# Kernel tuning notes

Hardware: AMD Instinct MI355X
Metric: run time of the kernel (lower is better)

Reference implementation:

```python
import jax, jax.numpy as jnp
import numpy as np


def _l2norm(x, axis):
    return x / jnp.maximum(jnp.linalg.norm(x, axis=axis, keepdims=True), 1e-12)


def setup_inputs() -> dict:
    key = jax.random.key(0)
    ks = jax.random.split(key, 16)
    N, D, F, TI, HD = 1000, 100, 100, 512, 128
    # binary doc-word membership masks, ~50 words per document
    masks = (jax.random.uniform(ks[0], (D, N)) < 0.05).astype(jnp.float32)
    # sparse symmetric normalized word-graph adjacency
    a = (jax.random.uniform(ks[1], (N, N)) < 0.01).astype(jnp.float32)
    adj = jnp.maximum(a, a.T) + jnp.eye(N, dtype=jnp.float32)
    dinv = 1.0 / jnp.sqrt(adj.sum(axis=1))
    train_adj = adj * dinv[:, None] * dinv[None, :]
    bows_vec = jax.random.normal(ks[2], (N, F), dtype=jnp.float32) * 0.1
    image_features = jax.random.normal(ks[3], (D, TI), dtype=jnp.float32)

    def sc(i, sh):
        return jax.random.normal(ks[i], sh, dtype=jnp.float32) * np.float32(1.0 / np.sqrt(sh[0]))

    return {
        'epoch': 3, 'epochs': 10,
        'train_adj': train_adj, 'masks': masks, 'bows_vec': bows_vec,
        'image_features': image_features,
        'W_g1': sc(4, (F, F)), 'W_g2': sc(5, (F, F)),
        'W_h1': sc(6, (F, F)), 'b_h1': jnp.zeros(F, jnp.float32),
        'W_h2': sc(7, (F, F)), 'b_h2': jnp.zeros(F, jnp.float32),
        'W_mu2': sc(8, (F, 1)), 'b_mu2': jnp.zeros(1, jnp.float32),
        'W_eta2': sc(9, (F, 1)), 'b_eta2': jnp.zeros(1, jnp.float32),
        'W_gamma2': sc(10, (F, 1)), 'b_gamma2': jnp.zeros(1, jnp.float32),
        'w_m': sc(11, (F, 1)), 'W_beta': sc(12, (F, 1)),
        'W_m1': sc(13, (TI, HD)), 'b_m1': jnp.zeros(HD, jnp.float32),
        'W_m2': sc(14, (HD, 1)), 'b_m2': jnp.zeros(1, jnp.float32),
    }


def reference(epoch, epochs, train_adj, masks, bows_vec, image_features,
              W_g1, W_g2, W_h1, b_h1, W_h2, b_h2,
              W_mu2, b_mu2, W_eta2, b_eta2, W_gamma2, b_gamma2,
              w_m, W_beta, W_m1, b_m1, W_m2, b_m2):
    N = train_adj.shape[0]
    # --- GcnNet: 2-layer GCN over word graph; doc embedding = masked mean pool ---
    H1 = jax.nn.relu(train_adj @ (bows_vec @ W_g1))        # [N,100]
    H = train_adj @ (H1 @ W_g2)                            # [N,100]
    cnt = masks.sum(axis=1, keepdims=True)                 # [D,1]
    H_p = (masks @ H) / jnp.maximum(cnt, 1.0)              # [D,100]

    H_eli = jax.nn.relu(jax.nn.relu(H @ W_h1 + b_h1) @ W_h2 + b_h2)
    H_eli_norm = _l2norm(H_eli, axis=1)                    # [N,100]

    mu = jax.nn.relu(H_p @ W_mu2 + b_mu2)                  # [D,1]
    # dropout disabled (eval mode)
    eta = jax.nn.relu(H_p @ W_eta2 + b_eta2)               # [D,1]
    gamma = jax.nn.relu(H_p @ W_gamma2 + b_gamma2)         # [D,1]

    sparsity = (epoch / epochs) * 0.3                      # python float (static)
    flat = w_m.reshape(-1)
    j = int(round(sparsity * flat.shape[0]))
    order = jnp.argsort(flat)                              # ascending; drop lowest j
    binary = jnp.zeros_like(flat).at[order[j:]].set(1.0)
    mask_ste = flat + jax.lax.stop_gradient(binary - flat) # forward==binary
    w_pruned = mask_ste.reshape(-1, 1) * W_beta            # [100,1]
    beta_ = _l2norm((H @ w_pruned)[:, 0], axis=0)          # [N]
    beta = masks @ beta_[:, None]                          # [D,1]

    Z_ = jax.nn.relu(H_eli_norm @ H_eli_norm.T)            # [N,N]

    # per-doc sum over distinct word pairs of h_i . h_j ; ||h||=1 so
    # sum_{a<b} h_a.h_b = (||sum_a h_a||^2 - k)/2 with k = #words in doc
    s = masks @ H_eli_norm                                 # [D,100]
    k = masks.sum(axis=1)                                  # [D]
    Z = jax.nn.relu(0.5 * (jnp.sum(s * s, axis=1) - k))[:, None]  # [D,1]

    # Z_event: per-doc [N,N] with entries at local positions p,q < k_i (p!=q)
    # (original indexes Z_ with LOCAL sorted positions 0..k_i-1; kept faithful)
    pos = jnp.arange(N)
    valid = (pos[None, :] < k[:, None]).astype(jnp.float32)       # [D,N]
    E = jnp.exp(-jnp.square(2.0 - 2.0 * Z_)) * (1.0 - jnp.eye(N)) # [N,N]
    Z_event = E[None, :, :] * valid[:, :, None] * valid[:, None, :]  # [D,N,N]

    lambda_texts = jax.nn.sigmoid(mu + beta + eta * jnp.exp(-gamma * Z))
    h_img = jax.nn.relu(image_features @ W_m1 + b_m1)
    lambda_imgs = h_img @ W_m2 + b_m2                      # MLP(512,128,1)
    lambda_total = jax.nn.sigmoid(lambda_texts + lambda_imgs)
    return (lambda_total, Z_, beta_, gamma, eta, Z_event, H)
```

## Files before the change

kernel.cpp:

```cpp
#include <hip/hip_runtime.h>
#include <hip/hip_bf16.h>

typedef __hip_bfloat16 bf;

#define NN   1000
#define DD   100
#define FF   100
#define TIF  512
#define HDD  128
#define EB   256
#define ACAP 96
#define MCAP 192

#define O_LAM 0
#define O_Z   100
#define O_B3  1000100
#define O_GAM 1001100
#define O_ETA 1001200
#define O_ZE  1001300
#define O_H   101001300

__device__ __forceinline__ float ldf(const void* p, int i, int F32){
  return F32 ? ((const float*)p)[i] : __bfloat162float(((const __hip_bfloat16*)p)[i]);
}

__device__ __forceinline__ float blk_red(float v, volatile float* red, int tid){
#pragma unroll
  for (int o=32;o>0;o>>=1) v += __shfl_down(v,o,64);
  if ((tid&63)==0) red[tid>>6]=v;
  __syncthreads();
  float r = red[0]+red[1];
  __syncthreads();
  return r;
}
__device__ __forceinline__ float blk_red4(float v, volatile float* red, int tid){
#pragma unroll
  for (int o=32;o>0;o>>=1) v += __shfl_down(v,o,64);
  if ((tid&63)==0) red[tid>>6]=v;
  __syncthreads();
  float r = red[0]+red[1]+red[2]+red[3];
  __syncthreads();
  return r;
}

__device__ __forceinline__ int sniffF32(const unsigned short* __restrict__ p, int tid){
  int lane = tid & 63;
  const ushort4* q = (const ushort4*)p;
  ushort4 a = q[lane*2], b = q[lane*2+1];
  int c = 0;
  c += (((a.x>>7)&0xFF)>=0xE0); c += (((a.y>>7)&0xFF)>=0xE0);
  c += (((a.z>>7)&0xFF)>=0xE0); c += (((a.w>>7)&0xFF)>=0xE0);
  c += (((b.x>>7)&0xFF)>=0xE0); c += (((b.y>>7)&0xFF)>=0xE0);
  c += (((b.z>>7)&0xFF)>=0xE0); c += (((b.w>>7)&0xFF)>=0xE0);
#pragma unroll
  for (int o=32;o>0;o>>=1) c += __shfl_xor(c,o,64);
  return c > 8;
}

__device__ __forceinline__ void zero_span(uint4* __restrict__ zb, long off, long cnt,
                                          int zi, int nzb, int tid, int bdim){
  long per = (cnt + nzb - 1)/nzb;
  long s = (long)zi*per; if (s>cnt) s=cnt;
  long e = s+per; if (e>cnt) e=cnt;
  uint4 z; z.x=z.y=z.z=z.w=0u;
  for (long i=off+s+tid; i<off+e; i+=bdim) zb[i]=z;
}

__global__ void k1_build(const void* __restrict__ A, const void* __restrict__ masks,
                         const void* __restrict__ wm, const void* __restrict__ Wbeta,
                         const void* __restrict__ img, const void* __restrict__ Wm1,
                         const void* __restrict__ bm1, const void* __restrict__ Wm2,
                         const void* __restrict__ bm2, const void* __restrict__ X,
                         const void* __restrict__ Wg1,
                         const int* epoch, const int* epochs,
                         int* a_idx, float* a_val, int* a_nnz,
                         int* m_idx, int* m_cnt, float* wpr, float* sumsq,
                         float* limg, int* flag, float* __restrict__ XW,
                         uint4* __restrict__ zb){
  int b = blockIdx.x; int lane = threadIdx.x;
  if (b >= NN+DD+1+DD+NN){ zero_span(zb, 0L, 8000000L, b-(NN+DD+1+DD+NN), 2048, lane, 64); return; }
  int F32 = sniffF32((const unsigned short*)X, lane);
  if (b < NN){
    int i=b, nn=0;
    for (int base=0;base<NN;base+=64){
      int c=base+lane; float v=0.f;
      if (c<NN) v=ldf(A, i*NN+c, F32);
      unsigned long long m=__ballot(v!=0.f);
      if (v!=0.f){
        int pos=nn+__popcll(m&((1ull<<lane)-1ull));
        if (pos<ACAP){ a_idx[i*ACAP+pos]=c; a_val[i*ACAP+pos]=v; }
      }
      nn+=__popcll(m);
    }
    if (lane==0) a_nnz[i]=min(nn,ACAP);
  } else if (b < NN+DD){
    int d=b-NN, nn=0;
    for (int base=0;base<NN;base+=64){
      int c=base+lane; float v=0.f;
      if (c<NN) v=ldf(masks, d*NN+c, F32);
      unsigned long long m=__ballot(v!=0.f);
      if (v!=0.f){
        int pos=nn+__popcll(m&((1ull<<lane)-1ull));
        if (pos<MCAP) m_idx[d*MCAP+pos]=c;
      }
      nn+=__popcll(m);
    }
    if (lane==0) m_cnt[d]=min(nn,MCAP);
  } else if (b == NN+DD){
    __shared__ float w[FF];
    for (int t=lane;t<FF;t+=64) w[t]=ldf(wm, t, F32);
    __syncthreads();
    float sp = 0.3f*(float)epoch[0]/(float)epochs[0];
    int j=(int)lroundf(sp*(float)FF);
    for (int t=lane;t<FF;t+=64){
      float v=w[t]; int r=0;
      for (int u=0;u<FF;u++){ float vu=w[u]; r += ((vu<v)||(vu==v && u<t)) ? 1 : 0; }
      wpr[t] = (r>=j)? ldf(Wbeta, t, F32) : 0.f;
    }
    if (lane==0){ sumsq[0]=0.f; flag[0]=F32; }
  } else if (b < NN+DD+1+DD){
    int d = b - (NN+DD+1);
    __shared__ float ir[TIF];
    for (int t=lane;t<TIF;t+=64) ir[t]=ldf(img, d*TIF+t, F32);
    __syncthreads();
    float acc=0.f;
    for (int h=lane; h<HDD; h+=64){
      float a=ldf(bm1, h, F32);
#pragma unroll 4
      for (int t=0;t<TIF;t++) a=fmaf(ir[t], ldf(Wm1, t*HDD+h, F32), a);
      acc = fmaf(fmaxf(a,0.f), ldf(Wm2, h, F32), acc);
    }
#pragma unroll
    for (int o=32;o>0;o>>=1) acc += __shfl_down(acc,o,64);
    if (lane==0) limg[d]=acc+ldf(bm2,0,F32);
  } else {
    int r = b - (NN+DD+1+DD);
    __shared__ float ar[FF];
    for (int t=lane;t<FF;t+=64) ar[t]=ldf(X, r*FF+t, F32);
    __syncthreads();
    for (int col=lane; col<FF; col+=64){
      float a=0.f;
#pragma unroll 4
      for (int c=0;c<FF;c++) a=fmaf(ar[c], ldf(Wg1, c*FF+col, F32), a);
      XW[r*FF+col]=a;
    }
  }
}

__global__ void k2_h1(const float* __restrict__ XW, const void* __restrict__ Wg2,
                      const int* flag, const int* __restrict__ a_idx,
                      const float* __restrict__ a_val, const int* __restrict__ a_nnz,
                      float* __restrict__ H1W, uint4* __restrict__ zb){
  int row=blockIdx.x, tx=threadIdx.x;
  if (row >= NN){ zero_span(zb, 8000000L, 5000000L, row-NN, 1280, tx, 128); return; }
  __shared__ int sidx[ACAP]; __shared__ float sval[ACAP]; __shared__ float t1[FF];
  int nn=a_nnz[row];
  for (int t=tx;t<nn;t+=128){ sidx[t]=a_idx[row*ACAP+t]; sval[t]=a_val[row*ACAP+t]; }
  __syncthreads();
  if (tx<FF){
    float a=0.f;
    for (int m=0;m<nn;m++) a=fmaf(sval[m], XW[sidx[m]*FF+tx], a);
    t1[tx]=fmaxf(a,0.f);
  }
  __syncthreads();
  int F32=flag[0];
  if (tx<FF){
    float s=0.f;
#pragma unroll 4
    for (int c=0;c<FF;c++) s=fmaf(t1[c], ldf(Wg2, c*FF+tx, F32), s);
    H1W[row*FF+tx]=s;
  }
}

__global__ void k3_h2(const float* __restrict__ H1W, const int* __restrict__ a_idx,
                      const float* __restrict__ a_val, const int* __restrict__ a_nnz,
                      const void* __restrict__ Wh1, const void* __restrict__ bh1,
                      const void* __restrict__ Wh2, const void* __restrict__ bh2,
                      const float* __restrict__ wpr, const int* flag,
                      float* __restrict__ Hh, float* __restrict__ Hn,
                      float* __restrict__ HnT, float* __restrict__ hw, float* sumsq,
                      float* __restrict__ outH, uint4* __restrict__ zb){
  int i=blockIdx.x, tx=threadIdx.x;
  if (i >= NN){ zero_span(zb, 13000000L, 5000000L, i-NN, 1280, tx, 128); return; }
  __shared__ int sidx[ACAP]; __shared__ float sval[ACAP];
  __shared__ float hr[FF], t1[FF];
  __shared__ float red[2];
  int nn=a_nnz[i];
  for (int t=tx;t<nn;t+=128){ sidx[t]=a_idx[i*ACAP+t]; sval[t]=a_val[i*ACAP+t]; }
  __syncthreads();
  if (tx<FF){
    float a=0.f;
    for (int m=0;m<nn;m++) a=fmaf(sval[m], H1W[sidx[m]*FF+tx], a);
    hr[tx]=a; Hh[i*FF+tx]=a; outH[i*FF+tx]=a;
  }
  __syncthreads();
  int F32=flag[0];
  if (tx<FF){
    float a=ldf(bh1, tx, F32);
#pragma unroll 4
    for (int c=0;c<FF;c++) a=fmaf(hr[c], ldf(Wh1, c*FF+tx, F32), a);
    t1[tx]=fmaxf(a,0.f);
  }
  __syncthreads();
  float hel=0.f;
  if (tx<FF){
    float s=ldf(bh2, tx, F32);
#pragma unroll 4
    for (int c=0;c<FF;c++) s=fmaf(t1[c], ldf(Wh2, c*FF+tx, F32), s);
    hel=fmaxf(s,0.f);
  }
  float phw = (tx<FF)? hr[tx]*wpr[tx] : 0.f;
  float rs2 = blk_red(hel*hel, red, tx);
  float rhw = blk_red(phw, red, tx);
  float rinv = 1.f/fmaxf(sqrtf(rs2), 1e-12f);
  if (tx<FF){ float v=hel*rinv; Hn[i*FF+tx]=v; HnT[tx*NN+i]=v; }
  if (tx==0){ hw[i]=rhw; atomicAdd(sumsq, rhw*rhw); }
}

__global__ __launch_bounds__(256) void k4_zdoc(const float* __restrict__ HnT,
                      const float* __restrict__ Hh, const float* __restrict__ Hn,
                      const float* __restrict__ hw, const float* __restrict__ sumsq,
                      const int* __restrict__ m_idx, const int* __restrict__ m_cnt,
                      const void* Wmu, const void* bmu, const void* Weta, const void* beta_b,
                      const void* Wgam, const void* bgam, const int* flag,
                      const float* __restrict__ limg,
                      float* __restrict__ out, float* __restrict__ Eblk,
                      uint4* __restrict__ zb){
  int b=blockIdx.x, tid=threadIdx.x;
  if (b >= 360){ zero_span(zb, 18000000L, 7000000L, b-360, 1792, tid, 256); return; }
  if (b < 256){
    int bi=(b&15)*64, bj=(b>>4)*64;
    __shared__ float At[FF*68], Bt[FF*68];
    for (int t=tid;t<FF*64;t+=256){
      int k=t>>6, ii=t&63;
      int gi=bi+ii, gj=bj+ii;
      At[k*68+ii] = (gi<NN)? HnT[k*NN+gi] : 0.f;
      Bt[k*68+ii] = (gj<NN)? HnT[k*NN+gj] : 0.f;
    }
    __syncthreads();
    int tx=tid&15, ty=tid>>4;
    float acc[4][4]={};
    for (int k=0;k<FF;k++){
      float4 av=*(float4*)&At[k*68+4*ty];
      float4 bv=*(float4*)&Bt[k*68+4*tx];
      float aa[4]={av.x,av.y,av.z,av.w};
      float bb[4]={bv.x,bv.y,bv.z,bv.w};
#pragma unroll
      for (int q=0;q<4;q++)
#pragma unroll
        for (int r=0;r<4;r++) acc[q][r]=fmaf(aa[q],bb[r],acc[q][r]);
    }
#pragma unroll
    for (int q=0;q<4;q++){
      int gi=bi+4*ty+q; if (gi>=NN) continue;
      float z[4];
#pragma unroll
      for (int r=0;r<4;r++) z[r]=fmaxf(acc[q][r],0.f);
      int gj0=bj+4*tx;
      if (gj0+3<NN){
        float4 zz; zz.x=z[0]; zz.y=z[1]; zz.z=z[2]; zz.w=z[3];
        *(float4*)&out[O_Z+(size_t)gi*NN+gj0]=zz;
      } else {
        for (int r=0;r<4;r++) if (gj0+r<NN) out[O_Z+(size_t)gi*NN+gj0+r]=z[r];
      }
      if (gi<EB && gj0<EB){
#pragma unroll
        for (int r=0;r<4;r++){
          int gj=gj0+r;
          float t2=2.f-2.f*z[r];
          Eblk[gi*EB+gj]=(gi==gj)?0.f:expf(-t2*t2);
        }
      }
    }
    return;
  }
  if (b >= 356){
    int i=(b-356)*256+tid;
    if (i<NN){
      float rinv=1.f/fmaxf(sqrtf(sumsq[0]),1e-12f);
      out[O_B3+i]=hw[i]*rinv;
    }
    return;
  }
  int d=b-256;
  int F32 = flag[0];
  __shared__ int sidx[MCAP]; __shared__ float red[4];
  int cnt=m_cnt[d];
  for (int t=tid;t<cnt;t+=256) sidx[t]=m_idx[d*MCAP+t];
  __syncthreads();
  float accH=0.f, accS=0.f;
  if (tid<FF) for (int m=0;m<cnt;m++){ int n=sidx[m]; accH+=Hh[n*FF+tid]; accS+=Hn[n*FF+tid]; }
  float Hp = accH/fmaxf((float)cnt,1.f);
  float pmu = (tid<FF)? Hp*ldf(Wmu, tid, F32)  : 0.f;
  float peta= (tid<FF)? Hp*ldf(Weta, tid, F32) : 0.f;
  float pgam= (tid<FF)? Hp*ldf(Wgam, tid, F32) : 0.f;
  float phw=0.f;
  for (int m=tid;m<cnt;m+=256) phw+=hw[sidx[m]];
  float rmu =blk_red4(pmu,red,tid);
  float reta=blk_red4(peta,red,tid);
  float rgam=blk_red4(pgam,red,tid);
  float rs2 =blk_red4(accS*accS,red,tid);
  float rhw =blk_red4(phw,red,tid);
  if (tid==0){
    float mu =fmaxf(rmu +ldf(bmu,0,F32),   0.f);
    float eta=fmaxf(reta+ldf(beta_b,0,F32),0.f);
    float gam=fmaxf(rgam+ldf(bgam,0,F32),  0.f);
    float Zd =fmaxf(0.5f*(rs2-(float)cnt), 0.f);
    float beta=rhw/fmaxf(sqrtf(sumsq[0]),1e-12f);
    float lt=1.f/(1.f+expf(-(mu+beta+eta*expf(-gam*Zd))));
    out[O_LAM+d]=1.f/(1.f+expf(-(lt+limg[d])));
    out[O_GAM+d]=gam;
    out[O_ETA+d]=eta;
  }
}

__global__ void k5_fill(const float* __restrict__ Eblk, const int* __restrict__ m_cnt,
                        float* __restrict__ outZE){
  int d=blockIdx.x; int k=m_cnt[d]; if (k>EB) k=EB;
  int kk=k*k;
  for (int idx=threadIdx.x; idx<kk; idx+=256){
    int i=idx/k, j=idx-i*k;
    float e=(i==j)?0.f:Eblk[i*EB+j];
    outZE[(size_t)d*1000000 + (size_t)i*1000 + j]=e;
  }
}

extern "C" void kernel_launch(void* const* d_in, const int* in_sizes, int n_in,
                              void* d_out, int out_size, void* d_ws, size_t ws_size,
                              hipStream_t stream) {
  const int* epoch  = (const int*)d_in[0];
  const int* epochs = (const int*)d_in[1];
  const void* A     = d_in[2];
  const void* masks = d_in[3];
  const void* X     = d_in[4];
  const void* img   = d_in[5];
  const void* Wg1   = d_in[6];
  const void* Wg2   = d_in[7];
  const void* Wh1   = d_in[8];
  const void* bh1   = d_in[9];
  const void* Wh2   = d_in[10];
  const void* bh2   = d_in[11];
  const void* Wmu   = d_in[12];
  const void* bmu   = d_in[13];
  const void* Weta  = d_in[14];
  const void* beta_b= d_in[15];
  const void* Wgam  = d_in[16];
  const void* bgam  = d_in[17];
  const void* wm    = d_in[18];
  const void* Wbeta = d_in[19];
  const void* Wm1   = d_in[20];
  const void* bm1   = d_in[21];
  const void* Wm2   = d_in[22];
  const void* bm2   = d_in[23];
  float* out = (float*)d_out;

  float* ws   = (float*)d_ws;
  float* XW   = ws;
  float* H1W  = XW  + 100000;
  float* Hh   = H1W + 100000;
  float* Hn   = Hh  + 100000;
  float* HnT  = Hn  + 100000;
  float* Eblk = HnT + 100000;
  float* a_val= Eblk+ 65536;
  int* a_idx  = (int*)(a_val + 96000);
  int* a_nnz  = a_idx + 96000;
  int* m_idx  = a_nnz + 1000;
  int* m_cnt  = m_idx + 19200;
  float* wpr  = (float*)(m_cnt + 100);
  float* hw   = wpr + 100;
  float* sumsq= hw + 1000;
  int* flag   = (int*)(sumsq + 4);
  float* limg = (float*)(flag + 4);

  uint4* zb = (uint4*)((char*)d_out + (size_t)O_ZE*4);

  hipLaunchKernelGGL(k1_build, dim3(NN+DD+1+DD+NN+2048), dim3(64), 0, stream,
                     A, masks, wm, Wbeta, img, Wm1, bm1, Wm2, bm2, X, Wg1,
                     epoch, epochs,
                     a_idx, a_val, a_nnz, m_idx, m_cnt, wpr, sumsq, limg, flag, XW, zb);
  hipLaunchKernelGGL(k2_h1, dim3(NN+1280), dim3(128), 0, stream,
                     XW, Wg2, flag, a_idx, a_val, a_nnz, H1W, zb);
  hipLaunchKernelGGL(k3_h2, dim3(NN+1280), dim3(128), 0, stream,
                     H1W, a_idx, a_val, a_nnz, Wh1, bh1, Wh2, bh2, wpr, flag,
                     Hh, Hn, HnT, hw, sumsq, out + O_H, zb);
  hipLaunchKernelGGL(k4_zdoc, dim3(360+1792), dim3(256), 0, stream,
                     HnT, Hh, Hn, hw, sumsq, m_idx, m_cnt,
                     Wmu, bmu, Weta, beta_b, Wgam, bgam, flag, limg,
                     out, Eblk, zb);
  hipLaunchKernelGGL(k5_fill, dim3(DD), dim3(256), 0, stream, Eblk, m_cnt, out + O_ZE);
}
```

Measured before the change: 667.9 us.

## Interleave zero-fill blocks with compute blocks and use nontemporal stores

Block indices in each kernel now alternate between compute work and zero-fill work for the large Z_event output. Before, all zero-fill blocks came after the compute blocks. The goal is to run memory-bound zeroing alongside compute from the start, so the tail is not dominated by zeroing. The zero stores also switch to nontemporal builtins to avoid polluting the cache. The index remapping has to cover exactly the same work set, and any mismatch there would be a bug.

New measurement: 646.6 us. -3.2%, faster.

```diff
diff --git a/kernel.cpp b/kernel.cpp
--- a/kernel.cpp
+++ b/kernel.cpp
@@ -2,6 +2,7 @@
 #include <hip/hip_bf16.h>
 
 typedef __hip_bfloat16 bf;
+typedef unsigned int u32x4 __attribute__((ext_vector_type(4)));
 
 #define NN   1000
 #define DD   100
@@ -57,13 +58,14 @@
   return c > 8;
 }
 
-__device__ __forceinline__ void zero_span(uint4* __restrict__ zb, long off, long cnt,
+__device__ __forceinline__ void zero_span(uint4* __restrict__ zb_, long off, long cnt,
                                           int zi, int nzb, int tid, int bdim){
+  u32x4* __restrict__ zb = (u32x4*)zb_;
   long per = (cnt + nzb - 1)/nzb;
   long s = (long)zi*per; if (s>cnt) s=cnt;
   long e = s+per; if (e>cnt) e=cnt;
-  uint4 z; z.x=z.y=z.z=z.w=0u;
-  for (long i=off+s+tid; i<off+e; i+=bdim) zb[i]=z;
+  u32x4 z = (u32x4)(0u,0u,0u,0u);
+  for (long i=off+s+tid; i<off+e; i+=bdim) __builtin_nontemporal_store(z, &zb[i]);
 }
 
 __global__ void k1_build(const void* __restrict__ A, const void* __restrict__ masks,
@@ -77,8 +79,12 @@
                          int* m_idx, int* m_cnt, float* wpr, float* sumsq,
                          float* limg, int* flag, float* __restrict__ XW,
                          uint4* __restrict__ zb){
-  int b = blockIdx.x; int lane = threadIdx.x;
-  if (b >= NN+DD+1+DD+NN){ zero_span(zb, 0L, 8000000L, b-(NN+DD+1+DD+NN), 2048, lane, 64); return; }
+  int bid = blockIdx.x; int lane = threadIdx.x;
+  int wi = -1, zi = -1;
+  if (bid < 4096){ if (bid & 1) zi = bid >> 1; else wi = bid >> 1; }
+  else wi = 2048 + (bid - 4096);
+  if (zi >= 0){ zero_span(zb, 0L, 8000000L, zi, 2048, lane, 64); return; }
+  int b = wi;
   int F32 = sniffF32((const unsigned short*)X, lane);
   if (b < NN){
     int i=b, nn=0;
@@ -151,8 +157,12 @@
                       const int* flag, const int* __restrict__ a_idx,
                       const float* __restrict__ a_val, const int* __restrict__ a_nnz,
                       float* __restrict__ H1W, uint4* __restrict__ zb){
-  int row=blockIdx.x, tx=threadIdx.x;
-  if (row >= NN){ zero_span(zb, 8000000L, 5000000L, row-NN, 1280, tx, 128); return; }
+  int bid=blockIdx.x, tx=threadIdx.x;
+  int wi=-1, zi=-1;
+  if (bid < 2000){ if (bid & 1) zi = bid >> 1; else wi = bid >> 1; }
+  else zi = 1000 + (bid - 2000);
+  if (zi >= 0){ zero_span(zb, 8000000L, 5000000L, zi, 1280, tx, 128); return; }
+  int row = wi;
   __shared__ int sidx[ACAP]; __shared__ float sval[ACAP]; __shared__ float t1[FF];
   int nn=a_nnz[row];
   for (int t=tx;t<nn;t+=128){ sidx[t]=a_idx[row*ACAP+t]; sval[t]=a_val[row*ACAP+t]; }
@@ -180,8 +190,12 @@
                       float* __restrict__ Hh, float* __restrict__ Hn,
                       float* __restrict__ HnT, float* __restrict__ hw, float* sumsq,
                       float* __restrict__ outH, uint4* __restrict__ zb){
-  int i=blockIdx.x, tx=threadIdx.x;
-  if (i >= NN){ zero_span(zb, 13000000L, 5000000L, i-NN, 1280, tx, 128); return; }
+  int bid=blockIdx.x, tx=threadIdx.x;
+  int wi=-1, zi=-1;
+  if (bid < 2000){ if (bid & 1) zi = bid >> 1; else wi = bid >> 1; }
+  else zi = 1000 + (bid - 2000);
+  if (zi >= 0){ zero_span(zb, 13000000L, 5000000L, zi, 1280, tx, 128); return; }
+  int i = wi;
   __shared__ int sidx[ACAP]; __shared__ float sval[ACAP];
   __shared__ float hr[FF], t1[FF];
   __shared__ float red[2];
@@ -226,8 +240,12 @@
                       const float* __restrict__ limg,
                       float* __restrict__ out, float* __restrict__ Eblk,
                       uint4* __restrict__ zb){
-  int b=blockIdx.x, tid=threadIdx.x;
-  if (b >= 360){ zero_span(zb, 18000000L, 7000000L, b-360, 1792, tid, 256); return; }
+  int bid=blockIdx.x, tid=threadIdx.x;
+  int wi=-1, zi=-1;
+  if (bid < 720){ if (bid & 1) zi = bid >> 1; else wi = bid >> 1; }
+  else zi = 360 + (bid - 720);
+  if (zi >= 0){ zero_span(zb, 18000000L, 7000000L, zi, 1792, tid, 256); return; }
+  int b = wi;
   if (b < 256){
     int bi=(b&15)*64, bj=(b>>4)*64;
     __shared__ float At[FF*68], Bt[FF*68];
```

## Fuse five kernels into one cooperative persistent kernel with grid syncs

Applied to the files above, without the earlier changes.

Replaces the five separate kernel launches with a single cooperative kernel of 512 blocks that runs each former stage as a phase separated by grid.sync, and spreads the zeroing of the large Z_event output across all phases. Zero-fill stores become nontemporal vector stores. Per-row work is remapped so that one wave or half-block handles each unit, and the Z_ tile GEMM loads K in two chunks to fit shared memory. The intent is to remove launch gaps and tail idling between kernels. The cost is grid-wide barrier overhead and lower parallelism per phase, since only 512 blocks now cover work that previously ran on up to about 4000 blocks.

After: 935.9 us. +40.1%, slower.

```diff
diff --git a/kernel.cpp b/kernel.cpp
--- a/kernel.cpp
+++ b/kernel.cpp
@@ -1,7 +1,11 @@
 #include <hip/hip_runtime.h>
 #include <hip/hip_bf16.h>
+#include <hip/hip_cooperative_groups.h>
+
+namespace cg = cooperative_groups;
 
 typedef __hip_bfloat16 bf;
+typedef unsigned int u32x4 __attribute__((ext_vector_type(4)));
 
 #define NN   1000
 #define DD   100
@@ -24,10 +28,16 @@
   return F32 ? ((const float*)p)[i] : __bfloat162float(((const __hip_bfloat16*)p)[i]);
 }
 
-__device__ __forceinline__ float blk_red(float v, volatile float* red, int tid){
+__device__ __forceinline__ void wave_lds_sync(){
+  asm volatile("s_waitcnt lgkmcnt(0)" ::: "memory");
+  __builtin_amdgcn_wave_barrier();
+  __builtin_amdgcn_sched_barrier(0);
+}
+
+__device__ __forceinline__ float blk_red_half(float v, volatile float* red, int tx){
 #pragma unroll
   for (int o=32;o>0;o>>=1) v += __shfl_down(v,o,64);
-  if ((tid&63)==0) red[tid>>6]=v;
+  if ((tx&63)==0) red[tx>>6]=v;
   __syncthreads();
   float r = red[0]+red[1];
   __syncthreads();
@@ -43,8 +53,7 @@
   return r;
 }
 
-__device__ __forceinline__ int sniffF32(const unsigned short* __restrict__ p, int tid){
-  int lane = tid & 63;
+__device__ __forceinline__ int sniffF32(const unsigned short* __restrict__ p, int lane){
   const ushort4* q = (const ushort4*)p;
   ushort4 a = q[lane*2], b = q[lane*2+1];
   int c = 0;
@@ -57,335 +66,344 @@
   return c > 8;
 }
 
-__device__ __forceinline__ void zero_span(uint4* __restrict__ zb, long off, long cnt,
+__device__ __forceinline__ void zero_span(uint4* __restrict__ zb_, long off, long cnt,
                                           int zi, int nzb, int tid, int bdim){
+  u32x4* __restrict__ zb = (u32x4*)zb_;
   long per = (cnt + nzb - 1)/nzb;
   long s = (long)zi*per; if (s>cnt) s=cnt;
   long e = s+per; if (e>cnt) e=cnt;
-  uint4 z; z.x=z.y=z.z=z.w=0u;
-  for (long i=off+s+tid; i<off+e; i+=bdim) zb[i]=z;
-}
-
-__global__ void k1_build(const void* __restrict__ A, const void* __restrict__ masks,
-                         const void* __restrict__ wm, const void* __restrict__ Wbeta,
-                         const void* __restrict__ img, const void* __restrict__ Wm1,
-                         const void* __restrict__ bm1, const void* __restrict__ Wm2,
-                         const void* __restrict__ bm2, const void* __restrict__ X,
-                         const void* __restrict__ Wg1,
-                         const int* epoch, const int* epochs,
-                         int* a_idx, float* a_val, int* a_nnz,
-                         int* m_idx, int* m_cnt, float* wpr, float* sumsq,
-                         float* limg, int* flag, float* __restrict__ XW,
-                         uint4* __restrict__ zb){
-  int b = blockIdx.x; int lane = threadIdx.x;
-  if (b >= NN+DD+1+DD+NN){ zero_span(zb, 0L, 8000000L, b-(NN+DD+1+DD+NN), 2048, lane, 64); return; }
-  int F32 = sniffF32((const unsigned short*)X, lane);
-  if (b < NN){
-    int i=b, nn=0;
-    for (int base=0;base<NN;base+=64){
-      int c=base+lane; float v=0.f;
-      if (c<NN) v=ldf(A, i*NN+c, F32);
-      unsigned long long m=__ballot(v!=0.f);
-      if (v!=0.f){
-        int pos=nn+__popcll(m&((1ull<<lane)-1ull));
-        if (pos<ACAP){ a_idx[i*ACAP+pos]=c; a_val[i*ACAP+pos]=v; }
+  u32x4 z = (u32x4)(0u,0u,0u,0u);
+  for (long i=off+s+tid; i<off+e; i+=bdim) __builtin_nontemporal_store(z, &zb[i]);
+}
+
+struct Params {
+  const void *A, *masks, *wm, *Wbeta, *img, *Wm1, *bm1, *Wm2, *bm2, *X;
+  const void *Wg1, *Wg2, *Wh1, *bh1, *Wh2, *bh2;
+  const void *Wmu, *bmu, *Weta, *beta_b, *Wgam, *bgam;
+  const int *epoch, *epochs;
+  int *a_idx, *a_nnz, *m_idx, *m_cnt, *flag;
+  float *a_val, *wpr, *sumsq, *limg;
+  float *XW, *H1W, *Hh, *Hn, *HnT, *hw, *Eblk;
+  float *out;
+  uint4 *zb;
+};
+
+__global__ __launch_bounds__(256, 2) void mega(Params p){
+  cg::grid_group grid = cg::this_grid();
+  __shared__ float smem[6800];
+  int bid = blockIdx.x;
+  int tid = threadIdx.x;
+
+  {
+    int w = tid>>6, lane = tid&63;
+    float* ws0 = smem + w*512;
+    int F32 = sniffF32((const unsigned short*)p.X, lane);
+#pragma unroll 1
+    for (int rd=0; rd<2; rd++){
+      int u = bid*4 + w + rd*2048;
+      if (u >= NN+DD+1+DD+NN) continue;
+      if (u < NN){
+        int i=u, nn=0;
+        for (int base=0;base<NN;base+=64){
+          int c=base+lane; float v=0.f;
+          if (c<NN) v=ldf(p.A, i*NN+c, F32);
+          unsigned long long m=__ballot(v!=0.f);
+          if (v!=0.f){
+            int pos=nn+__popcll(m&((1ull<<lane)-1ull));
+            if (pos<ACAP){ p.a_idx[i*ACAP+pos]=c; p.a_val[i*ACAP+pos]=v; }
+          }
+          nn+=__popcll(m);
+        }
+        if (lane==0) p.a_nnz[i]=min(nn,ACAP);
+      } else if (u < NN+DD){
+        int d=u-NN, nn=0;
+        for (int base=0;base<NN;base+=64){
+          int c=base+lane; float v=0.f;
+          if (c<NN) v=ldf(p.masks, d*NN+c, F32);
+          unsigned long long m=__ballot(v!=0.f);
+          if (v!=0.f){
+            int pos=nn+__popcll(m&((1ull<<lane)-1ull));
+            if (pos<MCAP) p.m_idx[d*MCAP+pos]=c;
+          }
+          nn+=__popcll(m);
+        }
+        if (lane==0) p.m_cnt[d]=min(nn,MCAP);
+      } else if (u == NN+DD){
+        for (int t=lane;t<FF;t+=64) ws0[t]=ldf(p.wm, t, F32);
+        wave_lds_sync();
+        float sp = 0.3f*(float)p.epoch[0]/(float)p.epochs[0];
+        int j=(int)lroundf(sp*(float)FF);
+        for (int t=lane;t<FF;t+=64){
+          float v=ws0[t]; int r=0;
+          for (int uu=0;uu<FF;uu++){ float vu=ws0[uu]; r += ((vu<v)||(vu==v && uu<t)) ? 1 : 0; }
+          p.wpr[t] = (r>=j)? ldf(p.Wbeta, t, F32) : 0.f;
+        }
+        if (lane==0){ p.sumsq[0]=0.f; p.flag[0]=F32; }
+      } else if (u < NN+DD+1+DD){
+        int d = u - (NN+DD+1);
+        for (int t=lane;t<TIF;t+=64) ws0[t]=ldf(p.img, d*TIF+t, F32);
+        wave_lds_sync();
+        float acc=0.f;
+        for (int h=lane; h<HDD; h+=64){
+          float a=ldf(p.bm1, h, F32);
+#pragma unroll 4
+          for (int t=0;t<TIF;t++) a=fmaf(ws0[t], ldf(p.Wm1, t*HDD+h, F32), a);
+          acc = fmaf(fmaxf(a,0.f), ldf(p.Wm2, h, F32), acc);
+        }
+#pragma unroll
+        for (int o=32;o>0;o>>=1) acc += __shfl_down(acc,o,64);
+        if (lane==0) p.limg[d]=acc+ldf(p.bm2,0,F32);
+      } else {
+        int r = u - (NN+DD+1+DD);
+        for (int t=lane;t<FF;t+=64) ws0[t]=ldf(p.X, r*FF+t, F32);
+        wave_lds_sync();
+        for (int col=lane; col<FF; col+=64){
+          float a=0.f;
+#pragma unroll 4
+          for (int c=0;c<FF;c++) a=fmaf(ws0[c], ldf(p.Wg1, c*FF+col, F32), a);
+          p.XW[r*FF+col]=a;
+        }
       }
-      nn+=__popcll(m);
-    }
-    if (lane==0) a_nnz[i]=min(nn,ACAP);
-  } else if (b < NN+DD){
-    int d=b-NN, nn=0;
-    for (int base=0;base<NN;base+=64){
-      int c=base+lane; float v=0.f;
-      if (c<NN) v=ldf(masks, d*NN+c, F32);
-      unsigned long long m=__ballot(v!=0.f);
-      if (v!=0.f){
-        int pos=nn+__popcll(m&((1ull<<lane)-1ull));
-        if (pos<MCAP) m_idx[d*MCAP+pos]=c;
+    }
+    zero_span(p.zb, 0L, 6250000L, bid, 512, tid, 256);
+  }
+  grid.sync();
+
+  {
+    int hb = tid>>7, tx = tid&127;
+    float* sm = smem + hb*512;
+    int*   sidx = (int*)sm;
+    float* sval = sm+96;
+    float* t1   = sm+192;
+    int row = bid*2+hb;
+    bool act = (bid<500);
+    int F32 = p.flag[0];
+    int nn=0;
+    if (act){
+      nn=p.a_nnz[row];
+      for (int t=tx;t<nn;t+=128){ sidx[t]=p.a_idx[row*ACAP+t]; sval[t]=p.a_val[row*ACAP+t]; }
+    }
+    __syncthreads();
+    if (act && tx<FF){
+      float a=0.f;
+      for (int m=0;m<nn;m++) a=fmaf(sval[m], p.XW[sidx[m]*FF+tx], a);
+      t1[tx]=fmaxf(a,0.f);
+    }
+    __syncthreads();
+    if (act && tx<FF){
+      float s=0.f;
+#pragma unroll 4
+      for (int c=0;c<FF;c++) s=fmaf(t1[c], ldf(p.Wg2, c*FF+tx, F32), s);
+      p.H1W[row*FF+tx]=s;
+    }
+    zero_span(p.zb, 6250000L, 6250000L, bid, 512, tid, 256);
+  }
+  grid.sync();
+
+  {
+    int hb = tid>>7, tx = tid&127;
+    float* sm = smem + hb*512;
+    int*   sidx = (int*)sm;
+    float* sval = sm+96;
+    float* hr   = sm+192;
+    float* t1   = sm+292;
+    volatile float* red = (volatile float*)(sm+392);
+    int i = bid*2+hb;
+    bool act = (bid<500);
+    int F32 = p.flag[0];
+    int nn=0;
+    if (act){
+      nn=p.a_nnz[i];
+      for (int t=tx;t<nn;t+=128){ sidx[t]=p.a_idx[i*ACAP+t]; sval[t]=p.a_val[i*ACAP+t]; }
+    }
+    __syncthreads();
+    if (act && tx<FF){
+      float a=0.f;
+      for (int m=0;m<nn;m++) a=fmaf(sval[m], p.H1W[sidx[m]*FF+tx], a);
+      hr[tx]=a; p.Hh[i*FF+tx]=a; p.out[(size_t)O_H+(size_t)i*FF+tx]=a;
+    }
+    __syncthreads();
+    if (act && tx<FF){
+      float a=ldf(p.bh1, tx, F32);
+#pragma unroll 4
+      for (int c=0;c<FF;c++) a=fmaf(hr[c], ldf(p.Wh1, c*FF+tx, F32), a);
+      t1[tx]=fmaxf(a,0.f);
+    }
+    __syncthreads();
+    float hel=0.f;
+    if (act && tx<FF){
+      float s=ldf(p.bh2, tx, F32);
+#pragma unroll 4
+      for (int c=0;c<FF;c++) s=fmaf(t1[c], ldf(p.Wh2, c*FF+tx, F32), s);
+      hel=fmaxf(s,0.f);
+    }
+    float phw = (act && tx<FF)? hr[tx]*p.wpr[tx] : 0.f;
+    float rs2 = blk_red_half(hel*hel, red, tx);
+    float rhw = blk_red_half(phw, red, tx);
+    if (act){
+      float rinv = 1.f/fmaxf(sqrtf(rs2), 1e-12f);
+      if (tx<FF){ float v=hel*rinv; p.Hn[i*FF+tx]=v; p.HnT[tx*NN+i]=v; }
+      if (tx==0){ p.hw[i]=rhw; atomicAdd(p.sumsq, rhw*rhw); }
+    }
+    zero_span(p.zb, 12500000L, 6250000L, bid, 512, tid, 256);
+  }
+  grid.sync();
+
+  {
+    int F32 = p.flag[0];
+    if (bid < 256){
+      int b=bid;
+      int bi=(b&15)*64, bj=(b>>4)*64;
+      float* At = smem;
+      float* Bt = smem+3400;
+      int tx=tid&15, ty=tid>>4;
+      float acc[4][4]={};
+#pragma unroll 1
+      for (int kc=0;kc<2;kc++){
+        __syncthreads();
+        for (int t=tid;t<50*64;t+=256){
+          int k=t>>6, ii=t&63;
+          int gi=bi+ii, gj=bj+ii;
+          At[k*68+ii] = (gi<NN)? p.HnT[(kc*50+k)*NN+gi] : 0.f;
+          Bt[k*68+ii] = (gj<NN)? p.HnT[(kc*50+k)*NN+gj] : 0.f;
+        }
+        __syncthreads();
+        for (int k=0;k<50;k++){
+          float4 av=*(float4*)&At[k*68+4*ty];
+          float4 bv=*(float4*)&Bt[k*68+4*tx];
+          float aa[4]={av.x,av.y,av.z,av.w};
+          float bb[4]={bv.x,bv.y,bv.z,bv.w};
+#pragma unroll
+          for (int q=0;q<4;q++)
+#pragma unroll
+            for (int r=0;r<4;r++) acc[q][r]=fmaf(aa[q],bb[r],acc[q][r]);
+        }
       }
-      nn+=__popcll(m);
-    }
-    if (lane==0) m_cnt[d]=min(nn,MCAP);
-  } else if (b == NN+DD){
-    __shared__ float w[FF];
-    for (int t=lane;t<FF;t+=64) w[t]=ldf(wm, t, F32);
-    __syncthreads();
-    float sp = 0.3f*(float)epoch[0]/(float)epochs[0];
-    int j=(int)lroundf(sp*(float)FF);
-    for (int t=lane;t<FF;t+=64){
-      float v=w[t]; int r=0;
-      for (int u=0;u<FF;u++){ float vu=w[u]; r += ((vu<v)||(vu==v && u<t)) ? 1 : 0; }
-      wpr[t] = (r>=j)? ldf(Wbeta, t, F32) : 0.f;
-    }
-    if (lane==0){ sumsq[0]=0.f; flag[0]=F32; }
-  } else if (b < NN+DD+1+DD){
-    int d = b - (NN+DD+1);
-    __shared__ float ir[TIF];
-    for (int t=lane;t<TIF;t+=64) ir[t]=ldf(img, d*TIF+t, F32);
-    __syncthreads();
-    float acc=0.f;
-    for (int h=lane; h<HDD; h+=64){
-      float a=ldf(bm1, h, F32);
-#pragma unroll 4
-      for (int t=0;t<TIF;t++) a=fmaf(ir[t], ldf(Wm1, t*HDD+h, F32), a);
-      acc = fmaf(fmaxf(a,0.f), ldf(Wm2, h, F32), acc);
-    }
-#pragma unroll
-    for (int o=32;o>0;o>>=1) acc += __shfl_down(acc,o,64);
-    if (lane==0) limg[d]=acc+ldf(bm2,0,F32);
-  } else {
-    int r = b - (NN+DD+1+DD);
-    __shared__ float ar[FF];
-    for (int t=lane;t<FF;t+=64) ar[t]=ldf(X, r*FF+t, F32);
-    __syncthreads();
-    for (int col=lane; col<FF; col+=64){
-      float a=0.f;
-#pragma unroll 4
-      for (int c=0;c<FF;c++) a=fmaf(ar[c], ldf(Wg1, c*FF+col, F32), a);
-      XW[r*FF+col]=a;
-    }
+#pragma unroll
+      for (int q=0;q<4;q++){
+        int gi=bi+4*ty+q; if (gi>=NN) continue;
+        float z[4];
+#pragma unroll
+        for (int r=0;r<4;r++) z[r]=fmaxf(acc[q][r],0.f);
+        int gj0=bj+4*tx;
+        if (gj0+3<NN){
+          float4 zz; zz.x=z[0]; zz.y=z[1]; zz.z=z[2]; zz.w=z[3];
+          *(float4*)&p.out[O_Z+(size_t)gi*NN+gj0]=zz;
+        } else {
+          for (int r=0;r<4;r++) if (gj0+r<NN) p.out[O_Z+(size_t)gi*NN+gj0+r]=z[r];
+        }
+        if (gi<EB && gj0<EB){
+#pragma unroll
+          for (int r=0;r<4;r++){
+            int gj=gj0+r;
+            float t2=2.f-2.f*z[r];
+            p.Eblk[gi*EB+gj]=(gi==gj)?0.f:expf(-t2*t2);
+          }
+        }
+      }
+    } else if (bid < 356){
+      int d=bid-256;
+      int* sidx=(int*)smem;
+      volatile float* red=(volatile float*)(smem+192);
+      int cnt=p.m_cnt[d];
+      for (int t=tid;t<cnt;t+=256) sidx[t]=p.m_idx[d*MCAP+t];
+      __syncthreads();
+      float accH=0.f, accS=0.f;
+      if (tid<FF) for (int m=0;m<cnt;m++){ int n=sidx[m]; accH+=p.Hh[n*FF+tid]; accS+=p.Hn[n*FF+tid]; }
+      float Hp = accH/fmaxf((float)cnt,1.f);
+      float pmu = (tid<FF)? Hp*ldf(p.Wmu, tid, F32)  : 0.f;
+      float peta= (tid<FF)? Hp*ldf(p.Weta, tid, F32) : 0.f;
+      float pgam= (tid<FF)? Hp*ldf(p.Wgam, tid, F32) : 0.f;
+      float phw=0.f;
+      for (int m=tid;m<cnt;m+=256) phw+=p.hw[sidx[m]];
+      float rmu =blk_red4(pmu,red,tid);
+      float reta=blk_red4(peta,red,tid);
+      float rgam=blk_red4(pgam,red,tid);
+      float rs2 =blk_red4(accS*accS,red,tid);
+      float rhw =blk_red4(phw,red,tid);
+      if (tid==0){
+        float mu =fmaxf(rmu +ldf(p.bmu,0,F32),   0.f);
+        float eta=fmaxf(reta+ldf(p.beta_b,0,F32),0.f);
+        float gam=fmaxf(rgam+ldf(p.bgam,0,F32),  0.f);
+        float Zd =fmaxf(0.5f*(rs2-(float)cnt), 0.f);
+        float beta=rhw/fmaxf(sqrtf(p.sumsq[0]),1e-12f);
+        float lt=1.f/(1.f+expf(-(mu+beta+eta*expf(-gam*Zd))));
+        p.out[O_LAM+d]=1.f/(1.f+expf(-(lt+p.limg[d])));
+        p.out[O_GAM+d]=gam;
+        p.out[O_ETA+d]=eta;
+      }
+    } else if (bid < 360){
+      int i=(bid-356)*256+tid;
+      if (i<NN){
+        float rinv=1.f/fmaxf(sqrtf(p.sumsq[0]),1e-12f);
+        p.out[O_B3+i]=p.hw[i]*rinv;
+      }
+    }
+    zero_span(p.zb, 18750000L, 6250000L, bid, 512, tid, 256);
   }
-}
-
-__global__ void k2_h1(const float* __restrict__ XW, const void* __restrict__ Wg2,
-                      const int* flag, const int* __restrict__ a_idx,
-                      const float* __restrict__ a_val, const int* __restrict__ a_nnz,
-                      float* __restrict__ H1W, uint4* __restrict__ zb){
-  int row=blockIdx.x, tx=threadIdx.x;
-  if (row >= NN){ zero_span(zb, 8000000L, 5000000L, row-NN, 1280, tx, 128); return; }
-  __shared__ int sidx[ACAP]; __shared__ float sval[ACAP]; __shared__ float t1[FF];
-  int nn=a_nnz[row];
-  for (int t=tx;t<nn;t+=128){ sidx[t]=a_idx[row*ACAP+t]; sval[t]=a_val[row*ACAP+t]; }
-  __syncthreads();
-  if (tx<FF){
-    float a=0.f;
-    for (int m=0;m<nn;m++) a=fmaf(sval[m], XW[sidx[m]*FF+tx], a);
-    t1[tx]=fmaxf(a,0.f);
-  }
-  __syncthreads();
-  int F32=flag[0];
-  if (tx<FF){
-    float s=0.f;
-#pragma unroll 4
-    for (int c=0;c<FF;c++) s=fmaf(t1[c], ldf(Wg2, c*FF+tx, F32), s);
-    H1W[row*FF+tx]=s;
-  }
-}
-
-__global__ void k3_h2(const float* __restrict__ H1W, const int* __restrict__ a_idx,
-                      const float* __restrict__ a_val, const int* __restrict__ a_nnz,
-                      const void* __restrict__ Wh1, const void* __restrict__ bh1,
-                      const void* __restrict__ Wh2, const void* __restrict__ bh2,
-                      const float* __restrict__ wpr, const int* flag,
-                      float* __restrict__ Hh, float* __restrict__ Hn,
-                      float* __restrict__ HnT, float* __restrict__ hw, float* sumsq,
-                      float* __restrict__ outH, uint4* __restrict__ zb){
-  int i=blockIdx.x, tx=threadIdx.x;
-  if (i >= NN){ zero_span(zb, 13000000L, 5000000L, i-NN, 1280, tx, 128); return; }
-  __shared__ int sidx[ACAP]; __shared__ float sval[ACAP];
-  __shared__ float hr[FF], t1[FF];
-  __shared__ float red[2];
-  int nn=a_nnz[i];
-  for (int t=tx;t<nn;t+=128){ sidx[t]=a_idx[i*ACAP+t]; sval[t]=a_val[i*ACAP+t]; }
-  __syncthreads();
-  if (tx<FF){
-    float a=0.f;
-    for (int m=0;m<nn;m++) a=fmaf(sval[m], H1W[sidx[m]*FF+tx], a);
-    hr[tx]=a; Hh[i*FF+tx]=a; outH[i*FF+tx]=a;
-  }
-  __syncthreads();
-  int F32=flag[0];
-  if (tx<FF){
-    float a=ldf(bh1, tx, F32);
-#pragma unroll 4
-    for (int c=0;c<FF;c++) a=fmaf(hr[c], ldf(Wh1, c*FF+tx, F32), a);
-    t1[tx]=fmaxf(a,0.f);
-  }
-  __syncthreads();
-  float hel=0.f;
-  if (tx<FF){
-    float s=ldf(bh2, tx, F32);
-#pragma unroll 4
-    for (int c=0;c<FF;c++) s=fmaf(t1[c], ldf(Wh2, c*FF+tx, F32), s);
-    hel=fmaxf(s,0.f);
-  }
-  float phw = (tx<FF)? hr[tx]*wpr[tx] : 0.f;
-  float rs2 = blk_red(hel*hel, red, tx);
-  float rhw = blk_red(phw, red, tx);
-  float rinv = 1.f/fmaxf(sqrtf(rs2), 1e-12f);
-  if (tx<FF){ float v=hel*rinv; Hn[i*FF+tx]=v; HnT[tx*NN+i]=v; }
-  if (tx==0){ hw[i]=rhw; atomicAdd(sumsq, rhw*rhw); }
-}
-
-__global__ __launch_bounds__(256) void k4_zdoc(const float* __restrict__ HnT,
-                      const float* __restrict__ Hh, const float* __restrict__ Hn,
-                      const float* __restrict__ hw, const float* __restrict__ sumsq,
-                      const int* __restrict__ m_idx, const int* __restrict__ m_cnt,
-                      const void* Wmu, const void* bmu, const void* Weta, const void* beta_b,
-                      const void* Wgam, const void* bgam, const int* flag,
-                      const float* __restrict__ limg,
-                      float* __restrict__ out, float* __restrict__ Eblk,
-                      uint4* __restrict__ zb){
-  int b=blockIdx.x, tid=threadIdx.x;
-  if (b >= 360){ zero_span(zb, 18000000L, 7000000L, b-360, 1792, tid, 256); return; }
-  if (b < 256){
-    int bi=(b&15)*64, bj=(b>>4)*64;
-    __shared__ float At[FF*68], Bt[FF*68];
-    for (int t=tid;t<FF*64;t+=256){
-      int k=t>>6, ii=t&63;
-      int gi=bi+ii, gj=bj+ii;
-      At[k*68+ii] = (gi<NN)? HnT[k*NN+gi] : 0.f;
-      Bt[k*68+ii] = (gj<NN)? HnT[k*NN+gj] : 0.f;
-    }
-    __syncthreads();
-    int tx=tid&15, ty=tid>>4;
-    float acc[4][4]={};
-    for (int k=0;k<FF;k++){
-      float4 av=*(float4*)&At[k*68+4*ty];
-      float4 bv=*(float4*)&Bt[k*68+4*tx];
-      float aa[4]={av.x,av.y,av.z,av.w};
-      float bb[4]={bv.x,bv.y,bv.z,bv.w};
-#pragma unroll
-      for (int q=0;q<4;q++)
-#pragma unroll
-        for (int r=0;r<4;r++) acc[q][r]=fmaf(aa[q],bb[r],acc[q][r]);
-    }
-#pragma unroll
-    for (int q=0;q<4;q++){
-      int gi=bi+4*ty+q; if (gi>=NN) continue;
-      float z[4];
-#pragma unroll
-      for (int r=0;r<4;r++) z[r]=fmaxf(acc[q][r],0.f);
-      int gj0=bj+4*tx;
-      if (gj0+3<NN){
-        float4 zz; zz.x=z[0]; zz.y=z[1]; zz.z=z[2]; zz.w=z[3];
-        *(float4*)&out[O_Z+(size_t)gi*NN+gj0]=zz;
-      } else {
-        for (int r=0;r<4;r++) if (gj0+r<NN) out[O_Z+(size_t)gi*NN+gj0+r]=z[r];
-      }
-      if (gi<EB && gj0<EB){
-#pragma unroll
-        for (int r=0;r<4;r++){
-          int gj=gj0+r;
-          float t2=2.f-2.f*z[r];
-          Eblk[gi*EB+gj]=(gi==gj)?0.f:expf(-t2*t2);
-        }
-      }
-    }
-    return;
-  }
-  if (b >= 356){
-    int i=(b-356)*256+tid;
-    if (i<NN){
-      float rinv=1.f/fmaxf(sqrtf(sumsq[0]),1e-12f);
-      out[O_B3+i]=hw[i]*rinv;
-    }
-    return;
-  }
-  int d=b-256;
-  int F32 = flag[0];
-  __shared__ int sidx[MCAP]; __shared__ float red[4];
-  int cnt=m_cnt[d];
-  for (int t=tid;t<cnt;t+=256) sidx[t]=m_idx[d*MCAP+t];
-  __syncthreads();
-  float accH=0.f, accS=0.f;
-  if (tid<FF) for (int m=0;m<cnt;m++){ int n=sidx[m]; accH+=Hh[n*FF+tid]; accS+=Hn[n*FF+tid]; }
-  float Hp = accH/fmaxf((float)cnt,1.f);
-  float pmu = (tid<FF)? Hp*ldf(Wmu, tid, F32)  : 0.f;
-  float peta= (tid<FF)? Hp*ldf(Weta, tid, F32) : 0.f;
-  float pgam= (tid<FF)? Hp*ldf(Wgam, tid, F32) : 0.f;
-  float phw=0.f;
-  for (int m=tid;m<cnt;m+=256) phw+=hw[sidx[m]];
-  float rmu =blk_red4(pmu,red,tid);
-  float reta=blk_red4(peta,red,tid);
-  float rgam=blk_red4(pgam,red,tid);
-  float rs2 =blk_red4(accS*accS,red,tid);
-  float rhw =blk_red4(phw,red,tid);
-  if (tid==0){
-    float mu =fmaxf(rmu +ldf(bmu,0,F32),   0.f);
-    float eta=fmaxf(reta+ldf(beta_b,0,F32),0.f);
-    float gam=fmaxf(rgam+ldf(bgam,0,F32),  0.f);
-    float Zd =fmaxf(0.5f*(rs2-(float)cnt), 0.f);
-    float beta=rhw/fmaxf(sqrtf(sumsq[0]),1e-12f);
-    float lt=1.f/(1.f+expf(-(mu+beta+eta*expf(-gam*Zd))));
-    out[O_LAM+d]=1.f/(1.f+expf(-(lt+limg[d])));
-    out[O_GAM+d]=gam;
-    out[O_ETA+d]=eta;
-  }
-}
-
-__global__ void k5_fill(const float* __restrict__ Eblk, const int* __restrict__ m_cnt,
-                        float* __restrict__ outZE){
-  int d=blockIdx.x; int k=m_cnt[d]; if (k>EB) k=EB;
-  int kk=k*k;
-  for (int idx=threadIdx.x; idx<kk; idx+=256){
-    int i=idx/k, j=idx-i*k;
-    float e=(i==j)?0.f:Eblk[i*EB+j];
-    outZE[(size_t)d*1000000 + (size_t)i*1000 + j]=e;
+  grid.sync();
+
+  if (bid < DD){
+    int d=bid; int k=p.m_cnt[d]; if (k>EB) k=EB;
+    int kk=k*k;
+    for (int idx=tid; idx<kk; idx+=256){
+      int i2=idx/k, j=idx-i2*k;
+      float e=(i2==j)?0.f:p.Eblk[i2*EB+j];
+      p.out[(size_t)O_ZE + (size_t)d*1000000 + (size_t)i2*1000 + j]=e;
+    }
   }
 }
 
 extern "C" void kernel_launch(void* const* d_in, const int* in_sizes, int n_in,
                               void* d_out, int out_size, void* d_ws, size_t ws_size,
                               hipStream_t stream) {
-  const int* epoch  = (const int*)d_in[0];
-  const int* epochs = (const int*)d_in[1];
-  const void* A     = d_in[2];
-  const void* masks = d_in[3];
-  const void* X     = d_in[4];
-  const void* img   = d_in[5];
-  const void* Wg1   = d_in[6];
-  const void* Wg2   = d_in[7];
-  const void* Wh1   = d_in[8];
-  const void* bh1   = d_in[9];
-  const void* Wh2   = d_in[10];
-  const void* bh2   = d_in[11];
-  const void* Wmu   = d_in[12];
-  const void* bmu   = d_in[13];
-  const void* Weta  = d_in[14];
-  const void* beta_b= d_in[15];
-  const void* Wgam  = d_in[16];
-  const void* bgam  = d_in[17];
-  const void* wm    = d_in[18];
-  const void* Wbeta = d_in[19];
-  const void* Wm1   = d_in[20];
-  const void* bm1   = d_in[21];
-  const void* Wm2   = d_in[22];
-  const void* bm2   = d_in[23];
-  float* out = (float*)d_out;
+  Params P;
+  P.epoch  = (const int*)d_in[0];
+  P.epochs = (const int*)d_in[1];
+  P.A      = d_in[2];
+  P.masks  = d_in[3];
+  P.X      = d_in[4];
+  P.img    = d_in[5];
+  P.Wg1    = d_in[6];
+  P.Wg2    = d_in[7];
+  P.Wh1    = d_in[8];
+  P.bh1    = d_in[9];
+  P.Wh2    = d_in[10];
+  P.bh2    = d_in[11];
+  P.Wmu    = d_in[12];
+  P.bmu    = d_in[13];
+  P.Weta   = d_in[14];
+  P.beta_b = d_in[15];
+  P.Wgam   = d_in[16];
+  P.bgam   = d_in[17];
+  P.wm     = d_in[18];
+  P.Wbeta  = d_in[19];
+  P.Wm1    = d_in[20];
+  P.bm1    = d_in[21];
+  P.Wm2    = d_in[22];
+  P.bm2    = d_in[23];
+  P.out    = (float*)d_out;
 
   float* ws   = (float*)d_ws;
-  float* XW   = ws;
-  float* H1W  = XW  + 100000;
-  float* Hh   = H1W + 100000;
-  float* Hn   = Hh  + 100000;
-  float* HnT  = Hn  + 100000;
-  float* Eblk = HnT + 100000;
-  float* a_val= Eblk+ 65536;
-  int* a_idx  = (int*)(a_val + 96000);
-  int* a_nnz  = a_idx + 96000;
-  int* m_idx  = a_nnz + 1000;
-  int* m_cnt  = m_idx + 19200;
-  float* wpr  = (float*)(m_cnt + 100);
-  float* hw   = wpr + 100;
-  float* sumsq= hw + 1000;
-  int* flag   = (int*)(sumsq + 4);
-  float* limg = (float*)(flag + 4);
-
-  uint4* zb = (uint4*)((char*)d_out + (size_t)O_ZE*4);
-
-  hipLaunchKernelGGL(k1_build, dim3(NN+DD+1+DD+NN+2048), dim3(64), 0, stream,
-                     A, masks, wm, Wbeta, img, Wm1, bm1, Wm2, bm2, X, Wg1,
-                     epoch, epochs,
-                     a_idx, a_val, a_nnz, m_idx, m_cnt, wpr, sumsq, limg, flag, XW, zb);
-  hipLaunchKernelGGL(k2_h1, dim3(NN+1280), dim3(128), 0, stream,
-                     XW, Wg2, flag, a_idx, a_val, a_nnz, H1W, zb);
-  hipLaunchKernelGGL(k3_h2, dim3(NN+1280), dim3(128), 0, stream,
-                     H1W, a_idx, a_val, a_nnz, Wh1, bh1, Wh2, bh2, wpr, flag,
-                     Hh, Hn, HnT, hw, sumsq, out + O_H, zb);
-  hipLaunchKernelGGL(k4_zdoc, dim3(360+1792), dim3(256), 0, stream,
-                     HnT, Hh, Hn, hw, sumsq, m_idx, m_cnt,
-                     Wmu, bmu, Weta, beta_b, Wgam, bgam, flag, limg,
-                     out, Eblk, zb);
-  hipLaunchKernelGGL(k5_fill, dim3(DD), dim3(256), 0, stream, Eblk, m_cnt, out + O_ZE);
-}
+  P.XW   = ws;
+  P.H1W  = P.XW  + 100000;
+  P.Hh   = P.H1W + 100000;
+  P.Hn   = P.Hh  + 100000;
+  P.HnT  = P.Hn  + 100000;
+  P.Eblk = P.HnT + 100000;
+  P.a_val= P.Eblk+ 65536;
+  P.a_idx= (int*)(P.a_val + 96000);
+  P.a_nnz= P.a_idx + 96000;
+  P.m_idx= P.a_nnz + 1000;
+  P.m_cnt= P.m_idx + 19200;
+  P.wpr  = (float*)(P.m_cnt + 100);
+  P.hw   = P.wpr + 100;
+  P.sumsq= P.hw + 1000;
+  P.flag = (int*)(P.sumsq + 4);
+  P.limg = (float*)(P.flag + 4);
+
+  P.zb = (uint4*)((char*)d_out + (size_t)O_ZE*4);
+
+  void* kargs[] = { (void*)&P };
+  hipLaunchCooperativeKernel((const void*)mega, dim3(512), dim3(256), kargs, 0, stream);
+}
```
